# Optimization experiments

Hardware: AMD Instinct MI355X
Metric: run time of the kernel (lower is better)

Reference implementation:

```python
import jax, jax.numpy as jnp
import numpy as np

G = 256        # graphs per batch
N = 256        # nodes per graph (max_n for dense padding)
D = 256        # node_hidden_dim
H = 8          # num_heads
EPS = 1e-5


def _layer_norm(h, g, b):
    mu = jnp.mean(h, axis=-1, keepdims=True)
    var = jnp.mean((h - mu) ** 2, axis=-1, keepdims=True)
    return (h - mu) * jax.lax.rsqrt(var + EPS) * g + b


def setup_inputs() -> dict:
    key = jax.random.key(0)
    ks = jax.random.split(key, 16)
    s = 0.02
    inp = {
        "x": jax.random.normal(ks[0], (G * N, D), dtype=jnp.float32),
        "batch": jnp.repeat(jnp.arange(G, dtype=jnp.int32), N),  # sorted segment ids
        "batch_CLS": jax.random.normal(ks[1], (G, 1, D), dtype=jnp.float32),
        "Wq": jax.random.normal(ks[2], (D, D), dtype=jnp.float32) * s,
        "bq": jnp.zeros((D,), jnp.float32),
        "Wk": jax.random.normal(ks[3], (D, D), dtype=jnp.float32) * s,
        "bk": jnp.zeros((D,), jnp.float32),
        "Wv": jax.random.normal(ks[4], (D, D), dtype=jnp.float32) * s,
        "bv": jnp.zeros((D,), jnp.float32),
        "Wo": jax.random.normal(ks[5], (D, D), dtype=jnp.float32) * s,
        "bo": jnp.zeros((D,), jnp.float32),
        "g0": jnp.ones((D,), jnp.float32),
        "beta0": jnp.zeros((D,), jnp.float32),
        "W1": jax.random.normal(ks[6], (D, 2 * D), dtype=jnp.float32) * s,
        "b1": jnp.zeros((2 * D,), jnp.float32),
        "W2": jax.random.normal(ks[7], (2 * D, D), dtype=jnp.float32) * s,
        "b2": jnp.zeros((D,), jnp.float32),
        "g1": jnp.ones((D,), jnp.float32),
        "beta1": jnp.zeros((D,), jnp.float32),
    }
    return inp


def reference(x, batch, batch_CLS, Wq, bq, Wk, bk, Wv, bv, Wo, bo,
              g0, beta0, W1, b1, W2, b2, g1, beta1):
    total = x.shape[0]
    batch = batch.astype(jnp.int32)

    # ---- to_dense_batch: scatter nodes into [G, N, D] padded tensor + mask
    counts = jax.ops.segment_sum(jnp.ones((total,), jnp.int32), batch, num_segments=G)
    start = jnp.concatenate([jnp.zeros((1,), jnp.int32), jnp.cumsum(counts)[:-1]])
    pos = jnp.arange(total, dtype=jnp.int32) - start[batch]  # position within graph
    x_dense = jnp.zeros((G, N, D), x.dtype).at[batch, pos].set(x)
    mask = jnp.zeros((G, N), bool).at[batch, pos].set(True)

    # ---- append CLS token per graph
    x_dense = jnp.concatenate([x_dense, batch_CLS], axis=1)            # [G, N+1, D]
    attn_mask = jnp.concatenate([mask, jnp.ones((G, 1), bool)], axis=1)  # [G, N+1]

    # ---- masked multi-head self-attention (split/cat pattern == head reshape)
    dh = D // H
    Q = (x_dense @ Wq + bq).reshape(G, N + 1, H, dh)
    K = (x_dense @ Wk + bk).reshape(G, N + 1, H, dh)
    V = (x_dense @ Wv + bv).reshape(G, N + 1, H, dh)
    scores = jnp.einsum('bqhd,bkhd->bhqk', Q, K) / np.sqrt(dh).astype(np.float32)
    inf_mask = jnp.where(attn_mask, 0.0, -1e9)[:, None, None, :]        # [G,1,1,N+1]
    A = jax.nn.softmax(scores + inf_mask, axis=-1)
    attn = jnp.einsum('bhqk,bkhd->bqhd', A, V).reshape(G, N + 1, D)
    attn = attn @ Wo + bo

    # ---- residual, split CLS back off, gather dense->sparse
    attn = attn + x_dense
    cls = attn[:, -1, :]                       # [G, D]
    nodes = attn[:, :-1, :][batch, pos]        # [total, D] (inverse of to_dense_batch)
    h = jnp.concatenate([nodes, cls], axis=0)  # [total + G, D]

    h = _layer_norm(h, g0, beta0)
    f = jax.nn.relu(h @ W1 + b1) @ W2 + b2
    out = _layer_norm(f + h, g1, beta1)
    return out
```

## Files before the change

kernel.cpp:

```cpp
#include <hip/hip_runtime.h>

typedef __attribute__((ext_vector_type(8))) short short8;
typedef __attribute__((ext_vector_type(8))) unsigned short ushort8;
typedef __attribute__((ext_vector_type(4))) unsigned short ushort4v;
typedef __attribute__((ext_vector_type(4))) float f32x4;
typedef __attribute__((ext_vector_type(2))) unsigned int uint2v;
typedef unsigned short ushort;
typedef unsigned int uint;

#define QSCALE 0.17677669529663687f

__device__ __forceinline__ ushort f2bf(float f) {
  union { float f; unsigned u; } a; a.f = f;
  unsigned r = a.u + 0x7fffu + ((a.u >> 16) & 1u);
  return (ushort)(r >> 16);
}
__device__ __forceinline__ float bf2f(ushort u) {
  union { uint u; float f; } a; a.u = ((uint)u) << 16; return a.f;
}
__device__ __forceinline__ uint cvtpk(float a, float b) {
  uint r; asm("v_cvt_pk_bf16_f32 %0, %1, %2" : "=v"(r) : "v"(a), "v"(b)); return r;
}

__device__ __forceinline__ void gload16(const void* g, void* l) {
  __builtin_amdgcn_global_load_lds((const __attribute__((address_space(1))) void*)g,
                                   (__attribute__((address_space(3))) void*)l, 16, 0, 0);
}

__device__ __forceinline__ uint xcd_swz(uint hwid, uint nwg) {
  const uint q8 = nwg >> 3, r8 = nwg & 7;
  const uint xcd = hwid & 7, i8 = hwid >> 3;
  return (xcd < r8 ? xcd * (q8 + 1) : r8 * (q8 + 1) + (xcd - r8) * q8) + i8;
}

__global__ __launch_bounds__(256) void seg_start_k(const int* __restrict__ batch,
                                                   int* __restrict__ start) {
  const int i = blockIdx.x * 256 + threadIdx.x;
  const int b = batch[i];
  if (i == 0 || batch[i - 1] != b) start[b] = i;
  if (i == 0) start[256] = 65536;
}

__global__ __launch_bounds__(256) void prep_w_k(
    const float* __restrict__ Wq, const float* __restrict__ Wk,
    const float* __restrict__ Wv, const float* __restrict__ Wo,
    const float* __restrict__ W1, const float* __restrict__ W2,
    ushort* __restrict__ Wt) {
  const int w = blockIdx.y;
  const float* src; ushort* dst; int Kd, Nd; float sc = 1.0f;
  switch (w) {
    case 0: src = Wq; dst = Wt;          Kd = 256; Nd = 256; sc = QSCALE; break;
    case 1: src = Wk; dst = Wt + 65536;  Kd = 256; Nd = 256; break;
    case 2: src = Wv; dst = Wt + 131072; Kd = 256; Nd = 256; break;
    case 3: src = Wo; dst = Wt + 196608; Kd = 256; Nd = 256; break;
    case 4: src = W1; dst = Wt + 262144; Kd = 256; Nd = 512; break;
    default: src = W2; dst = Wt + 393216; Kd = 512; Nd = 256; break;
  }
  const int e = blockIdx.x * 256 + threadIdx.x;
  if (e < Kd * Nd) {
    const int k = e / Nd, n = e - k * Nd;
    dst[n * Kd + k] = f2bf(src[e] * sc);
  }
}

__global__ __launch_bounds__(256) void pack_xd_k(
    const float* __restrict__ x, const float* __restrict__ cls,
    const int* __restrict__ start, ushort* __restrict__ xd) {
  const size_t idx = (((size_t)blockIdx.x << 8) + threadIdx.x) << 3;
  const int row = (int)(idx >> 8);
  const int col = (int)(idx & 255);
  const int g = row / 257, n = row - g * 257;
  const int sg = start[g], cn = start[g + 1] - sg;
  float4 a, b;
  if (n < cn) {
    const float* src = x + (((size_t)(sg + n)) << 8) + col;
    a = ((const float4*)src)[0]; b = ((const float4*)src)[1];
  } else if (n == 256) {
    const float* src = cls + (((size_t)g) << 8) + col;
    a = ((const float4*)src)[0]; b = ((const float4*)src)[1];
  } else {
    a.x = a.y = a.z = a.w = 0.f; b = a;
  }
  ushort8 o;
  o[0] = f2bf(a.x); o[1] = f2bf(a.y); o[2] = f2bf(a.z); o[3] = f2bf(a.w);
  o[4] = f2bf(b.x); o[5] = f2bf(b.y); o[6] = f2bf(b.z); o[7] = f2bf(b.w);
  *(ushort8*)(xd + idx) = o;
}

template<int EPI>
__device__ __forceinline__ void gemm_a_body(
    const ushort* __restrict__ A, const ushort* __restrict__ Bt,
    int N, int K,
    const float* __restrict__ b0, const float* __restrict__ b1, const float* __restrict__ b2,
    ushort* __restrict__ o0, ushort* __restrict__ o1, ushort* __restrict__ o2,
    float* __restrict__ of32, const ushort* __restrict__ resid,
    const int* __restrict__ start) {
  __shared__ __align__(16) char As[16384];
  __shared__ __align__(16) char Bs[16384];
  const int tid = threadIdx.x, lane = tid & 63, wid = tid >> 6;
  const int hi = lane >> 4, lc = lane & 15;
  const int wm = wid >> 1, wn = wid & 1;

  const uint nx = gridDim.x, ny = gridDim.y;
  const uint hwid = blockIdx.y * nx + blockIdx.x;
  const uint wg = xcd_swz(hwid, nx * ny);
  const int bx = wg / ny, by = wg % ny;

  const int m0 = bx * 128;
  const int z = (EPI == 0) ? (by >> 1) : 0;
  const int ncol0 = (EPI == 0) ? (by & 1) * 128 : by * 128;
  const ushort* Bz = (EPI == 0) ? Bt + (size_t)z * 65536 : Bt;
  const float* bias = (EPI == 0) ? (z == 0 ? b0 : (z == 1 ? b1 : b2)) : b0;
  const float bmul = (EPI == 0 && z == 0) ? QSCALE : 1.0f;
  ushort* obf = (EPI == 0) ? (z == 0 ? o0 : (z == 1 ? o1 : o2)) : o0;

  f32x4 acc[4][4];
#pragma unroll
  for (int a = 0; a < 4; ++a)
#pragma unroll
    for (int b = 0; b < 4; ++b) acc[a][b] = (f32x4)0.0f;

  for (int kt = 0; kt < K; kt += 64) {
#pragma unroll
    for (int r = 0; r < 4; ++r) {
      const int L = (r * 256 + tid) * 16;
      const int row = L >> 7;
      const int cb = (L & 127) ^ ((row & 7) << 4);
      gload16(A + (size_t)(m0 + row) * K + kt + (cb >> 1), As + L);
    }
#pragma unroll
    for (int r = 0; r < 4; ++r) {
      const int L = (r * 256 + tid) * 16;
      const int row = L >> 7;
      const int cb = (L & 127) ^ ((row & 7) << 4);
      gload16(Bz + (size_t)(ncol0 + row) * K + kt + (cb >> 1), Bs + L);
    }
    asm volatile("s_waitcnt vmcnt(0)" ::: "memory");
    __syncthreads();
#pragma unroll
    for (int ks = 0; ks < 2; ++ks) {
      short8 af[4], bfr[4];
      const int cB = (ks * 32 + hi * 8) * 2;
#pragma unroll
      for (int t = 0; t < 4; ++t) {
        const int rA = wm * 64 + t * 16 + lc;
        af[t] = *(const short8*)(As + (rA << 7) + (cB ^ ((rA & 7) << 4)));
        const int rB = wn * 64 + t * 16 + lc;
        bfr[t] = *(const short8*)(Bs + (rB << 7) + (cB ^ ((rB & 7) << 4)));
      }
#pragma unroll
      for (int mt = 0; mt < 4; ++mt)
#pragma unroll
        for (int nt = 0; nt < 4; ++nt)
          acc[mt][nt] = __builtin_amdgcn_mfma_f32_16x16x32_bf16(af[mt], bfr[nt], acc[mt][nt], 0, 0, 0);
    }
    __syncthreads();
  }

#pragma unroll
  for (int mt = 0; mt < 4; ++mt)
#pragma unroll
    for (int i = 0; i < 4; ++i) {
      const int m = m0 + wm * 64 + mt * 16 + hi * 4 + i;
      size_t r2 = (size_t)m;
      bool wr = true;
      if constexpr (EPI == 4) {
        const int gg = m / 257, nr = m - gg * 257;
        const int sg = start[gg], cn = start[gg + 1] - sg;
        if (nr < cn) r2 = (size_t)(sg + nr);
        else if (nr == 256) r2 = (size_t)(65536 + gg);
        else wr = false;
      }
#pragma unroll
      for (int nt = 0; nt < 4; ++nt) {
        const int n = ncol0 + wn * 64 + nt * 16 + lc;
        if constexpr (EPI == 0) {
          obf[(size_t)m * N + n] = f2bf(acc[mt][nt][i] + bias[n] * bmul);
        } else if constexpr (EPI == 2) {
          obf[(size_t)m * N + n] = f2bf(fmaxf(acc[mt][nt][i] + bias[n], 0.0f));
        } else if constexpr (EPI == 4) {
          if (wr) {
            const float v = acc[mt][nt][i] + bias[n] + bf2f(resid[((size_t)m << 8) + n]);
            obf[(r2 << 8) + n] = f2bf(v);
          }
        } else {
          const float v = acc[mt][nt][i] + bias[n] + bf2f(resid[((size_t)m << 8) + n]);
          if constexpr (EPI == 6) obf[((size_t)m << 8) + n] = f2bf(v);
          else of32[((size_t)m << 8) + n] = v;
        }
      }
    }
}

__global__ __launch_bounds__(256) void gemm_qkv(
    const ushort* A, const ushort* Bt, const float* bq, const float* bk, const float* bv,
    ushort* Q, ushort* K, ushort* V) {
  gemm_a_body<0>(A, Bt, 256, 256, bq, bk, bv, Q, K, V, nullptr, nullptr, nullptr);
}
__global__ __launch_bounds__(256) void gemm_ffn1(
    const ushort* A, const ushort* Bt, const float* b1, ushort* t16) {
  gemm_a_body<2>(A, Bt, 512, 256, b1, nullptr, nullptr, t16, nullptr, nullptr,
                 nullptr, nullptr, nullptr);
}
__global__ __launch_bounds__(256) void gemm_wo(
    const ushort* A, const ushort* Bt, const float* bo,
    ushort* hpre16, const ushort* resid, const int* start) {
  gemm_a_body<4>(A, Bt, 256, 256, bo, nullptr, nullptr, hpre16, nullptr, nullptr,
                 nullptr, resid, start);
}
__global__ __launch_bounds__(256) void gemm_ffn2(
    const ushort* A, const ushort* Bt, const float* b2,
    float* out, const ushort* resid) {
  gemm_a_body<5>(A, Bt, 256, 512, b2, nullptr, nullptr, nullptr, nullptr, nullptr,
                 out, resid, nullptr);
}
__global__ __launch_bounds__(256) void gemm_ffn2b(
    const ushort* A, const ushort* Bt, const float* b2,
    ushort* fh16, const ushort* resid) {
  gemm_a_body<6>(A, Bt, 256, 512, b2, nullptr, nullptr, fh16, nullptr, nullptr,
                 nullptr, resid, nullptr);
}

template<int IN_BF, int OUT_BF>
__global__ __launch_bounds__(512) void ln_k(const void* __restrict__ in,
                                            const float* __restrict__ gamma,
                                            const float* __restrict__ beta,
                                            void* __restrict__ outp) {
  const int lane = threadIdx.x & 63, wid = threadIdx.x >> 6;
  const size_t r = (size_t)blockIdx.x * 8 + wid;
  float f[4];
  if constexpr (IN_BF) {
    const ushort4v v = *(const ushort4v*)((const ushort*)in + (r << 8) + lane * 4);
    f[0] = bf2f(v[0]); f[1] = bf2f(v[1]); f[2] = bf2f(v[2]); f[3] = bf2f(v[3]);
  } else {
    const float4 v = *(const float4*)((const float*)in + (r << 8) + lane * 4);
    f[0] = v.x; f[1] = v.y; f[2] = v.z; f[3] = v.w;
  }
  float s = (f[0] + f[1]) + (f[2] + f[3]);
  float ss = (f[0] * f[0] + f[1] * f[1]) + (f[2] * f[2] + f[3] * f[3]);
#pragma unroll
  for (int m = 1; m < 64; m <<= 1) {
    s += __shfl_xor(s, m); ss += __shfl_xor(ss, m);
  }
  const float mu = s * (1.0f / 256.0f);
  const float rs = rsqrtf(ss * (1.0f / 256.0f) - mu * mu + 1e-5f);
  const float4 gv = *(const float4*)(gamma + lane * 4);
  const float4 bv = *(const float4*)(beta + lane * 4);
  float o[4];
  o[0] = (f[0] - mu) * rs * gv.x + bv.x;
  o[1] = (f[1] - mu) * rs * gv.y + bv.y;
  o[2] = (f[2] - mu) * rs * gv.z + bv.z;
  o[3] = (f[3] - mu) * rs * gv.w + bv.w;
  if constexpr (OUT_BF) {
    ushort4v u;
    u[0] = f2bf(o[0]); u[1] = f2bf(o[1]); u[2] = f2bf(o[2]); u[3] = f2bf(o[3]);
    *(ushort4v*)((ushort*)outp + (r << 8) + lane * 4) = u;
  } else {
    float4 u; u.x = o[0]; u.y = o[1]; u.z = o[2]; u.w = o[3];
    *(float4*)((float*)outp + (r << 8) + lane * 4) = u;
  }
}

#define KSTR 40
#define VSTR 296
#define PSTR 104
#define OSTR 40
__global__ __launch_bounds__(512) void attn_k(
    const ushort* __restrict__ Q, const ushort* Kb,
    const ushort* __restrict__ Vb, const int* __restrict__ start,
    ushort* O) {
  __shared__ __align__(16) ushort Ks[272 * KSTR];
  __shared__ __align__(16) ushort Vt[32 * VSTR];
  __shared__ __align__(16) ushort Pb[8][16 * PSTR];
  const int tid = threadIdx.x, lane = tid & 63, wid = tid >> 6;
  const int hi = lane >> 4, lo = lane & 15;
  const uint wg = xcd_swz(blockIdx.x, 2048);
  const int g = wg >> 3, h = wg & 7;
  const int cnt = start[g + 1] - start[g];
  const size_t base = ((size_t)g * 257) * 256 + h * 32;

  for (int n = tid; n < 272; n += 512) {
    const bool rv = (n < cnt) || (n == 256);
    if (n < 257 && rv) {
      const ushort* src = Kb + base + ((size_t)n << 8);
#pragma unroll
      for (int j = 0; j < 4; ++j)
        *(ushort8*)(Ks + n * KSTR + j * 8) = *(const ushort8*)(src + j * 8);
    } else {
      const ushort8 zz = (ushort8)0;
#pragma unroll
      for (int j = 0; j < 4; ++j) *(ushort8*)(Ks + n * KSTR + j * 8) = zz;
    }
  }
  for (int u = tid; u < 576; u += 512) {
    const int npair = u % 144;
    const int d0 = (u / 144) * 8;
    const int n0 = npair * 2;
    const bool rv0 = (n0 < cnt) || (n0 == 256);
    const bool rv1 = (n0 + 1 < cnt) || (n0 + 1 == 256);
    ushort8 a8 = (ushort8)0, b8 = (ushort8)0;
    if (n0 < 257 && rv0) a8 = *(const ushort8*)(Vb + base + ((size_t)n0 << 8) + d0);
    if (n0 + 1 < 257 && rv1) b8 = *(const ushort8*)(Vb + base + ((size_t)(n0 + 1) << 8) + d0);
#pragma unroll
    for (int j = 0; j < 8; ++j)
      *(uint*)(Vt + (d0 + j) * VSTR + n0) = (uint)a8[j] | ((uint)b8[j] << 16);
  }
  __syncthreads();

  for (int qt = wid; qt < 17; qt += 8) {
    const int qr = qt * 16 + lo;
    const int qc = qr < 257 ? qr : 256;
    const short8 qf = *(const short8*)(Q + base + ((size_t)qc << 8) + hi * 8);
    ushort* Pw = Pb[wid];

    float den = -(float)(271 - cnt);
    f32x4 ot0 = (f32x4)0.0f, ot1 = (f32x4)0.0f;

#pragma unroll
    for (int ph = 0; ph < 3; ++ph) {
      const int nb = ph * 96;
      const int ktEnd = (ph == 2) ? 17 : ph * 6 + 6;
#pragma unroll
      for (int kt = ph * 6; kt < ktEnd; ++kt) {
        const short8 kf = *(const short8*)(Ks + (kt * 16 + lo) * KSTR + hi * 8);
        const f32x4 st = __builtin_amdgcn_mfma_f32_16x16x32_bf16(kf, qf, (f32x4)0.0f, 0, 0, 0);
        const float e0 = __expf(st[0]), e1 = __expf(st[1]);
        const float e2 = __expf(st[2]), e3 = __expf(st[3]);
        den += (e0 + e1) + (e2 + e3);
        uint2v w; w[0] = cvtpk(e0, e1); w[1] = cvtpk(e2, e3);
        *(uint2v*)(Pw + lo * PSTR + (kt * 16 + hi * 4 - nb)) = w;
      }
      if (ph == 2) {
        uint2v z0; z0[0] = 0u; z0[1] = 0u;
        *(uint2v*)(Pw + lo * PSTR + (80 + hi * 4)) = z0;
      }
      asm volatile("s_waitcnt lgkmcnt(0)" ::: "memory");
      __builtin_amdgcn_sched_barrier(0);
      __builtin_amdgcn_s_setprio(1);
#pragma unroll
      for (int ks = ph * 3; ks < ph * 3 + 3; ++ks) {
        const short8 pbf = *(const short8*)(Pw + lo * PSTR + (ks * 32 + hi * 8 - nb));
        const short8 va0 = *(const short8*)(Vt + lo * VSTR + ks * 32 + hi * 8);
        const short8 va1 = *(const short8*)(Vt + (16 + lo) * VSTR + ks * 32 + hi * 8);
        ot0 = __builtin_amdgcn_mfma_f32_16x16x32_bf16(va0, pbf, ot0, 0, 0, 0);
        ot1 = __builtin_amdgcn_mfma_f32_16x16x32_bf16(va1, pbf, ot1, 0, 0, 0);
      }
      __builtin_amdgcn_s_setprio(0);
      __builtin_amdgcn_sched_barrier(0);
    }

    den += __shfl_xor(den, 16);
    den += __shfl_xor(den, 32);
    const float inv = 1.0f / den;

    {
      const uint w0 = cvtpk(ot0[0] * inv, ot0[1] * inv);
      const uint w1 = cvtpk(ot0[2] * inv, ot0[3] * inv);
      const uint w2 = cvtpk(ot1[0] * inv, ot1[1] * inv);
      const uint w3 = cvtpk(ot1[2] * inv, ot1[3] * inv);
      ushort* ob = Pw + lo * OSTR + hi * 4;
      *(uint*)(ob + 0) = w0;
      *(uint*)(ob + 2) = w1;
      *(uint*)(ob + 16) = w2;
      *(uint*)(ob + 18) = w3;
    }
    asm volatile("s_waitcnt lgkmcnt(0)" ::: "memory");
    __builtin_amdgcn_sched_barrier(0);
    {
      const int r = lane >> 2;
      const int q2 = qt * 16 + r;
      const ushort8 ov = *(const ushort8*)(Pw + r * OSTR + (lane & 3) * 8);
      if (q2 < 257)
        *(ushort8*)(O + base + ((size_t)q2 << 8) + (lane & 3) * 8) = ov;
    }
    __builtin_amdgcn_sched_barrier(0);
  }
}

extern "C" void kernel_launch(void* const* d_in, const int* in_sizes, int n_in,
                              void* d_out, int out_size, void* d_ws, size_t ws_size,
                              hipStream_t stream) {
  (void)in_sizes; (void)n_in; (void)out_size;
  const float* x     = (const float*)d_in[0];
  const int*   batch = (const int*)d_in[1];
  const float* cls   = (const float*)d_in[2];
  const float* Wq    = (const float*)d_in[3];
  const float* bq    = (const float*)d_in[4];
  const float* Wk    = (const float*)d_in[5];
  const float* bk    = (const float*)d_in[6];
  const float* Wv    = (const float*)d_in[7];
  const float* bv    = (const float*)d_in[8];
  const float* Wo    = (const float*)d_in[9];
  const float* bo    = (const float*)d_in[10];
  const float* g0    = (const float*)d_in[11];
  const float* beta0 = (const float*)d_in[12];
  const float* W1    = (const float*)d_in[13];
  const float* b1    = (const float*)d_in[14];
  const float* W2    = (const float*)d_in[15];
  const float* b2    = (const float*)d_in[16];
  const float* g1    = (const float*)d_in[17];
  const float* beta1 = (const float*)d_in[18];

  char* ws = (char*)d_ws;
  int*    start = (int*)ws;
  ushort* Wt    = (ushort*)(ws + 4096);
  char*   sbase = ws + 1052672;
  ushort* Qb    = (ushort*)(sbase);
  ushort* Kb2   = (ushort*)(sbase + 33685504);
  ushort* Vb2   = (ushort*)(sbase + 67371008);
  ushort* fh16  = (ushort*)(sbase + 101056512);
  ushort* hpre16 = Qb;
  ushort* h16   = Vb2;
  ushort* tmid  = Qb;
  ushort* xd    = (ushort*)d_out;
  float*  out   = (float*)d_out;
  const bool big_ws = ws_size >= (size_t)135794688;

  seg_start_k<<<256, 256, 0, stream>>>(batch, start);
  prep_w_k<<<dim3(512, 6), 256, 0, stream>>>(Wq, Wk, Wv, Wo, W1, W2, Wt);
  pack_xd_k<<<8224, 256, 0, stream>>>(x, cls, start, xd);
  gemm_qkv<<<dim3(514, 6), 256, 0, stream>>>(xd, Wt, bq, bk, bv, Qb, Kb2, Vb2);
  attn_k<<<2048, 512, 0, stream>>>(Qb, Kb2, Vb2, start, Kb2);
  gemm_wo<<<dim3(514, 2), 256, 0, stream>>>(Kb2, Wt + 196608, bo, hpre16, xd, start);
  ln_k<1, 1><<<8224, 512, 0, stream>>>(hpre16, g0, beta0, h16);
  gemm_ffn1<<<dim3(514, 4), 256, 0, stream>>>(h16, Wt + 262144, b1, tmid);
  if (big_ws) {
    gemm_ffn2b<<<dim3(514, 2), 256, 0, stream>>>(tmid, Wt + 393216, b2, fh16, h16);
    ln_k<1, 0><<<8224, 512, 0, stream>>>(fh16, g1, beta1, out);
  } else {
    gemm_ffn2<<<dim3(514, 2), 256, 0, stream>>>(tmid, Wt + 393216, b2, out, h16);
    ln_k<0, 0><<<8224, 512, 0, stream>>>(out, g1, beta1, out);
  }
}
```

Baseline: 265.3 us.

## Process two query tiles per wave in attention and fold log2e into Q scale

Each wave in the attention kernel now handles a pair of 16-row query tiles, reusing every K fragment and V fragment load across both tiles. The P staging buffer is reshaped into smaller phases of 64 keys, with a 32-row buffer per wave. Query weights are prescaled by log2(e), so exp2f can replace __expf. The aim is fewer LDS reads per MFMA and more independent MFMA work per wave. In exchange, register use rises, and with 9 query pairs across 8 waves one wave does double work, which creates load imbalance (previously 17 tiles across 8 waves).

```diff
diff --git a/kernel.cpp b/kernel.cpp
--- a/kernel.cpp
+++ b/kernel.cpp
@@ -9,6 +9,7 @@
 typedef unsigned int uint;
 
 #define QSCALE 0.17677669529663687f
+#define QS2F (0.17677669529663687f * 1.4426950408889634f)
 
 __device__ __forceinline__ ushort f2bf(float f) {
   union { float f; unsigned u; } a; a.f = f;
@@ -49,7 +50,7 @@
   const int w = blockIdx.y;
   const float* src; ushort* dst; int Kd, Nd; float sc = 1.0f;
   switch (w) {
-    case 0: src = Wq; dst = Wt;          Kd = 256; Nd = 256; sc = QSCALE; break;
+    case 0: src = Wq; dst = Wt;          Kd = 256; Nd = 256; sc = QS2F; break;
     case 1: src = Wk; dst = Wt + 65536;  Kd = 256; Nd = 256; break;
     case 2: src = Wv; dst = Wt + 131072; Kd = 256; Nd = 256; break;
     case 3: src = Wo; dst = Wt + 196608; Kd = 256; Nd = 256; break;
@@ -111,7 +112,7 @@
   const int ncol0 = (EPI == 0) ? (by & 1) * 128 : by * 128;
   const ushort* Bz = (EPI == 0) ? Bt + (size_t)z * 65536 : Bt;
   const float* bias = (EPI == 0) ? (z == 0 ? b0 : (z == 1 ? b1 : b2)) : b0;
-  const float bmul = (EPI == 0 && z == 0) ? QSCALE : 1.0f;
+  const float bmul = (EPI == 0 && z == 0) ? QS2F : 1.0f;
   ushort* obf = (EPI == 0) ? (z == 0 ? o0 : (z == 1 ? o1 : o2)) : o0;
 
   f32x4 acc[4][4];
@@ -263,7 +264,7 @@
 
 #define KSTR 40
 #define VSTR 296
-#define PSTR 104
+#define PSTR 72
 #define OSTR 40
 __global__ __launch_bounds__(512) void attn_k(
     const ushort* __restrict__ Q, const ushort* Kb,
@@ -271,7 +272,7 @@
     ushort* O) {
   __shared__ __align__(16) ushort Ks[272 * KSTR];
   __shared__ __align__(16) ushort Vt[32 * VSTR];
-  __shared__ __align__(16) ushort Pb[8][16 * PSTR];
+  __shared__ __align__(16) ushort Pb[8][32 * PSTR];
   const int tid = threadIdx.x, lane = tid & 63, wid = tid >> 6;
   const int hi = lane >> 4, lo = lane & 15;
   const uint wg = xcd_swz(blockIdx.x, 2048);
@@ -307,71 +308,102 @@
   }
   __syncthreads();
 
-  for (int qt = wid; qt < 17; qt += 8) {
-    const int qr = qt * 16 + lo;
-    const int qc = qr < 257 ? qr : 256;
-    const short8 qf = *(const short8*)(Q + base + ((size_t)qc << 8) + hi * 8);
-    ushort* Pw = Pb[wid];
-
-    float den = -(float)(271 - cnt);
-    f32x4 ot0 = (f32x4)0.0f, ot1 = (f32x4)0.0f;
-
-#pragma unroll
-    for (int ph = 0; ph < 3; ++ph) {
-      const int nb = ph * 96;
-      const int ktEnd = (ph == 2) ? 17 : ph * 6 + 6;
-#pragma unroll
-      for (int kt = ph * 6; kt < ktEnd; ++kt) {
+  for (int qp = wid; qp < 9; qp += 8) {
+    const int qt0 = qp * 2, qt1 = qp * 2 + 1;
+    const int qr0 = qt0 * 16 + lo, qr1 = qt1 * 16 + lo;
+    const int qc0 = qr0 < 257 ? qr0 : 256;
+    const int qc1 = qr1 < 257 ? qr1 : 256;
+    const short8 qf0 = *(const short8*)(Q + base + ((size_t)qc0 << 8) + hi * 8);
+    const short8 qf1 = *(const short8*)(Q + base + ((size_t)qc1 << 8) + hi * 8);
+    ushort* Pw0 = Pb[wid];
+    ushort* Pw1 = Pb[wid] + 16 * PSTR;
+
+    float den0 = -(float)(271 - cnt);
+    float den1 = den0;
+    f32x4 o00 = (f32x4)0.0f, o01 = (f32x4)0.0f;
+    f32x4 o10 = (f32x4)0.0f, o11 = (f32x4)0.0f;
+
+#pragma unroll
+    for (int ph = 0; ph < 5; ++ph) {
+      const int ktB = ph * 4;
+      const int ktE = (ph * 4 + 4 < 17) ? ph * 4 + 4 : 17;
+      const int nb = ph * 64;
+#pragma unroll
+      for (int kt = ktB; kt < ktE; ++kt) {
         const short8 kf = *(const short8*)(Ks + (kt * 16 + lo) * KSTR + hi * 8);
-        const f32x4 st = __builtin_amdgcn_mfma_f32_16x16x32_bf16(kf, qf, (f32x4)0.0f, 0, 0, 0);
-        const float e0 = __expf(st[0]), e1 = __expf(st[1]);
-        const float e2 = __expf(st[2]), e3 = __expf(st[3]);
-        den += (e0 + e1) + (e2 + e3);
-        uint2v w; w[0] = cvtpk(e0, e1); w[1] = cvtpk(e2, e3);
-        *(uint2v*)(Pw + lo * PSTR + (kt * 16 + hi * 4 - nb)) = w;
-      }
-      if (ph == 2) {
+        const f32x4 s0 = __builtin_amdgcn_mfma_f32_16x16x32_bf16(kf, qf0, (f32x4)0.0f, 0, 0, 0);
+        const f32x4 s1 = __builtin_amdgcn_mfma_f32_16x16x32_bf16(kf, qf1, (f32x4)0.0f, 0, 0, 0);
+        const float a0 = exp2f(s0[0]), a1 = exp2f(s0[1]), a2 = exp2f(s0[2]), a3 = exp2f(s0[3]);
+        den0 += (a0 + a1) + (a2 + a3);
+        uint2v w0; w0[0] = cvtpk(a0, a1); w0[1] = cvtpk(a2, a3);
+        *(uint2v*)(Pw0 + lo * PSTR + (kt * 16 + hi * 4 - nb)) = w0;
+        const float b0 = exp2f(s1[0]), b1 = exp2f(s1[1]), b2 = exp2f(s1[2]), b3 = exp2f(s1[3]);
+        den1 += (b0 + b1) + (b2 + b3);
+        uint2v w1; w1[0] = cvtpk(b0, b1); w1[1] = cvtpk(b2, b3);
+        *(uint2v*)(Pw1 + lo * PSTR + (kt * 16 + hi * 4 - nb)) = w1;
+      }
+      if (ph == 4) {
         uint2v z0; z0[0] = 0u; z0[1] = 0u;
-        *(uint2v*)(Pw + lo * PSTR + (80 + hi * 4)) = z0;
+        *(uint2v*)(Pw0 + lo * PSTR + (16 + hi * 4)) = z0;
+        *(uint2v*)(Pw1 + lo * PSTR + (16 + hi * 4)) = z0;
       }
       asm volatile("s_waitcnt lgkmcnt(0)" ::: "memory");
       __builtin_amdgcn_sched_barrier(0);
       __builtin_amdgcn_s_setprio(1);
-#pragma unroll
-      for (int ks = ph * 3; ks < ph * 3 + 3; ++ks) {
-        const short8 pbf = *(const short8*)(Pw + lo * PSTR + (ks * 32 + hi * 8 - nb));
+      const int ksB = ph * 2;
+      const int ksE = (ph * 2 + 2 < 9) ? ph * 2 + 2 : 9;
+#pragma unroll
+      for (int ks = ksB; ks < ksE; ++ks) {
         const short8 va0 = *(const short8*)(Vt + lo * VSTR + ks * 32 + hi * 8);
         const short8 va1 = *(const short8*)(Vt + (16 + lo) * VSTR + ks * 32 + hi * 8);
-        ot0 = __builtin_amdgcn_mfma_f32_16x16x32_bf16(va0, pbf, ot0, 0, 0, 0);
-        ot1 = __builtin_amdgcn_mfma_f32_16x16x32_bf16(va1, pbf, ot1, 0, 0, 0);
+        const short8 p0 = *(const short8*)(Pw0 + lo * PSTR + (ks * 32 + hi * 8 - nb));
+        const short8 p1 = *(const short8*)(Pw1 + lo * PSTR + (ks * 32 + hi * 8 - nb));
+        o00 = __builtin_amdgcn_mfma_f32_16x16x32_bf16(va0, p0, o00, 0, 0, 0);
+        o01 = __builtin_amdgcn_mfma_f32_16x16x32_bf16(va1, p0, o01, 0, 0, 0);
+        o10 = __builtin_amdgcn_mfma_f32_16x16x32_bf16(va0, p1, o10, 0, 0, 0);
+        o11 = __builtin_amdgcn_mfma_f32_16x16x32_bf16(va1, p1, o11, 0, 0, 0);
       }
       __builtin_amdgcn_s_setprio(0);
       __builtin_amdgcn_sched_barrier(0);
     }
 
-    den += __shfl_xor(den, 16);
-    den += __shfl_xor(den, 32);
-    const float inv = 1.0f / den;
+    den0 += __shfl_xor(den0, 16); den0 += __shfl_xor(den0, 32);
+    den1 += __shfl_xor(den1, 16); den1 += __shfl_xor(den1, 32);
+    const float inv0 = 1.0f / den0;
+    const float inv1 = 1.0f / den1;
 
     {
-      const uint w0 = cvtpk(ot0[0] * inv, ot0[1] * inv);
-      const uint w1 = cvtpk(ot0[2] * inv, ot0[3] * inv);
-      const uint w2 = cvtpk(ot1[0] * inv, ot1[1] * inv);
-      const uint w3 = cvtpk(ot1[2] * inv, ot1[3] * inv);
-      ushort* ob = Pw + lo * OSTR + hi * 4;
+      const uint w0 = cvtpk(o00[0] * inv0, o00[1] * inv0);
+      const uint w1 = cvtpk(o00[2] * inv0, o00[3] * inv0);
+      const uint w2 = cvtpk(o01[0] * inv0, o01[1] * inv0);
+      const uint w3 = cvtpk(o01[2] * inv0, o01[3] * inv0);
+      ushort* ob = Pw0 + lo * OSTR + hi * 4;
       *(uint*)(ob + 0) = w0;
       *(uint*)(ob + 2) = w1;
       *(uint*)(ob + 16) = w2;
       *(uint*)(ob + 18) = w3;
+      const uint x0 = cvtpk(o10[0] * inv1, o10[1] * inv1);
+      const uint x1 = cvtpk(o10[2] * inv1, o10[3] * inv1);
+      const uint x2 = cvtpk(o11[0] * inv1, o11[1] * inv1);
+      const uint x3 = cvtpk(o11[2] * inv1, o11[3] * inv1);
+      ushort* ob1 = Pw1 + lo * OSTR + hi * 4;
+      *(uint*)(ob1 + 0) = x0;
+      *(uint*)(ob1 + 2) = x1;
+      *(uint*)(ob1 + 16) = x2;
+      *(uint*)(ob1 + 18) = x3;
     }
     asm volatile("s_waitcnt lgkmcnt(0)" ::: "memory");
     __builtin_amdgcn_sched_barrier(0);
     {
       const int r = lane >> 2;
-      const int q2 = qt * 16 + r;
-      const ushort8 ov = *(const ushort8*)(Pw + r * OSTR + (lane & 3) * 8);
-      if (q2 < 257)
-        *(ushort8*)(O + base + ((size_t)q2 << 8) + (lane & 3) * 8) = ov;
+      const ushort8 ov0 = *(const ushort8*)(Pw0 + r * OSTR + (lane & 3) * 8);
+      const int q20 = qt0 * 16 + r;
+      if (q20 < 257)
+        *(ushort8*)(O + base + ((size_t)q20 << 8) + (lane & 3) * 8) = ov0;
+      const ushort8 ov1 = *(const ushort8*)(Pw1 + r * OSTR + (lane & 3) * 8);
+      const int q21 = qt1 * 16 + r;
+      if (q21 < 257)
+        *(ushort8*)(O + base + ((size_t)q21 << 8) + (lane & 3) * 8) = ov1;
     }
     __builtin_amdgcn_sched_barrier(0);
   }
```

Result: no change. 267.9 us (+1.0%).
